# Performance work log

Measured on AMD Instinct MI355X. Metric: run time of the kernel, lower is better.

Reference implementation:

```python
import jax, jax.numpy as jnp
import numpy as np

B, H, W, C = 64, 224, 224, 32

def setup_inputs() -> dict:
    key = jax.random.key(0)
    k1, k2, k3 = jax.random.split(key, 3)
    x = jax.random.normal(k1, (B, H, W, C), dtype=jnp.float32)
    # Dense(4) params: kernel [C, 4], bias [4] (keras glorot-ish scale)
    W_cls = jax.random.normal(k2, (C, 4), dtype=jnp.float32) * (1.0 / np.sqrt(C))
    b_cls = jax.random.normal(k3, (4,), dtype=jnp.float32) * 0.01
    return {"x": x, "W_cls": W_cls, "b_cls": b_cls}

def reference(x, W_cls, b_cls):
    # mean-pool over spatial dims -> [B, C]
    mean_features = jnp.mean(x, axis=(1, 2))
    logits = mean_features @ W_cls + b_cls          # [B, 4]
    k = jnp.argmax(logits, axis=-1)                 # [B] int32
    # tf.image.rot90 rotates counter-clockwise; jnp.rot90(axes=(1,2)) matches.
    # Vectorized routing: materialize all 4 rotations, gather per-sample by k.
    rots = jnp.stack([
        x,
        jnp.rot90(x, 1, axes=(1, 2)),
        jnp.rot90(x, 2, axes=(1, 2)),
        jnp.rot90(x, 3, axes=(1, 2)),
    ], axis=0)                                      # [4, B, H, W, C]
    out = rots[k, jnp.arange(x.shape[0])]           # [B, H, W, C]
    return out
```

## Files before the change

kernel.cpp:

```cpp
#include <hip/hip_runtime.h>
#include <math.h>

#define B_  64
#define H_  224
#define W_  224
#define C_  32
#define HW_ (H_ * W_)

__global__ __launch_bounds__(256) void sum_kernel(const float* __restrict__ x,
                                                  float* __restrict__ sums) {
    const int blk   = blockIdx.x;
    const int b     = blk / 98;
    const int chunk = blk % 98;
    const int t     = threadIdx.x;
    const int c4    = t & 7;
    const int prow  = t >> 3;

    const float4* xb = (const float4*)(x + (size_t)b * HW_ * C_);
    const int pos0 = chunk * 512 + prow;

    float4 acc = make_float4(0.f, 0.f, 0.f, 0.f);
#pragma unroll
    for (int it = 0; it < 16; ++it) {
        const int pos = pos0 + it * 32;
        const float4 v = xb[(size_t)pos * 8 + c4];
        acc.x += v.x; acc.y += v.y; acc.z += v.z; acc.w += v.w;
    }

    __shared__ float4 s[256];
    s[t] = acc;
    __syncthreads();
#pragma unroll
    for (int stride = 128; stride >= 8; stride >>= 1) {
        if (t < stride) {
            const float4 o = s[t + stride];
            s[t].x += o.x; s[t].y += o.y; s[t].z += o.z; s[t].w += o.w;
        }
        __syncthreads();
    }
    if (t < 8) {
        const float4 v = s[t];
        atomicAdd(&sums[b * C_ + t * 4 + 0], v.x);
        atomicAdd(&sums[b * C_ + t * 4 + 1], v.y);
        atomicAdd(&sums[b * C_ + t * 4 + 2], v.z);
        atomicAdd(&sums[b * C_ + t * 4 + 3], v.w);
    }
}

__global__ void classify_kernel(const float* __restrict__ sums,
                                const float* __restrict__ Wc,
                                const float* __restrict__ bc,
                                int* __restrict__ kk) {
    const int b = threadIdx.x;
    if (b >= B_) return;
    float m[C_];
    const float inv = 1.0f / (float)HW_;
#pragma unroll
    for (int c = 0; c < C_; ++c) m[c] = sums[b * C_ + c] * inv;

    float best = -INFINITY;
    int bi = 0;
#pragma unroll
    for (int j = 0; j < 4; ++j) {
        float l = bc[j];
#pragma unroll
        for (int c = 0; c < C_; ++c) l += m[c] * Wc[c * 4 + j];
        if (l > best) { best = l; bi = j; }
    }
    kk[b] = bi;
}

__global__ __launch_bounds__(256) void rotate_kernel(const float* __restrict__ x,
                                                     const int* __restrict__ kk,
                                                     float* __restrict__ out) {
    const int blk = blockIdx.x;
    const int b = blk / H_;
    const int i = blk % H_;
    const int k = kk[b];

    const float4* xb = (const float4*)(x + (size_t)b * HW_ * C_);
    float4* ob = (float4*)(out + ((size_t)b * HW_ + (size_t)i * W_) * C_);

    const int t = threadIdx.x;
#pragma unroll
    for (int rep = 0; rep < 7; ++rep) {
        const int idx = rep * 256 + t;
        const int j  = idx >> 3;
        const int c4 = idx & 7;
        int si, sj;
        switch (k) {
            case 0:  si = i;          sj = j;          break;
            case 1:  si = j;          sj = W_ - 1 - i; break;
            case 2:  si = H_ - 1 - i; sj = W_ - 1 - j; break;
            default: si = H_ - 1 - j; sj = i;          break;
        }
        ob[idx] = xb[((size_t)si * W_ + sj) * 8 + c4];
    }
}

extern "C" void kernel_launch(void* const* d_in, const int* in_sizes, int n_in,
                              void* d_out, int out_size, void* d_ws, size_t ws_size,
                              hipStream_t stream) {
    const float* x   = (const float*)d_in[0];
    const float* Wc  = (const float*)d_in[1];
    const float* bc  = (const float*)d_in[2];
    float* out       = (float*)d_out;

    float* sums = (float*)d_ws;
    int*   kk   = (int*)((char*)d_ws + B_ * C_ * 4);

    hipMemsetAsync(sums, 0, B_ * C_ * sizeof(float), stream);

    sum_kernel<<<B_ * 98, 256, 0, stream>>>(x, sums);
    classify_kernel<<<1, 64, 0, stream>>>(sums, Wc, bc, kk);
    rotate_kernel<<<B_ * H_, 256, 0, stream>>>(x, kk, out);
}
```

Measured before the change: 751.1 us.

## Tile rotate kernel through shared memory and reverse batch order

Rotation now loads 16x16 pixel tiles into shared memory and writes them out rotated, so global reads and writes are both contiguous runs of pixels instead of row-strided single-pixel accesses. Batches are also processed in reverse order so the data the sum kernel touched last may still be in cache. This adds a barrier and possible LDS bank conflicts.

```diff
diff --git a/kernel.cpp b/kernel.cpp
--- a/kernel.cpp
+++ b/kernel.cpp
@@ -6,6 +6,8 @@
 #define W_  224
 #define C_  32
 #define HW_ (H_ * W_)
+#define T_  16
+#define TILES_ (W_ / T_)
 
 __global__ __launch_bounds__(256) void sum_kernel(const float* __restrict__ x,
                                                   float* __restrict__ sums) {
@@ -73,28 +75,54 @@
 __global__ __launch_bounds__(256) void rotate_kernel(const float* __restrict__ x,
                                                      const int* __restrict__ kk,
                                                      float* __restrict__ out) {
-    const int blk = blockIdx.x;
-    const int b = blk / H_;
-    const int i = blk % H_;
-    const int k = kk[b];
+    const int blk  = blockIdx.x;
+    const int b    = (B_ - 1) - blk / (TILES_ * TILES_);
+    const int trem = blk % (TILES_ * TILES_);
+    const int ti   = trem / TILES_;
+    const int tj   = trem % TILES_;
+    const int i0   = ti * T_;
+    const int j0   = tj * T_;
+    const int k    = kk[b];
+
+    int sr0, sc0;
+    switch (k) {
+        case 0:  sr0 = i0;           sc0 = j0;           break;
+        case 1:  sr0 = j0;           sc0 = W_ - T_ - i0; break;
+        case 2:  sr0 = H_ - T_ - i0; sc0 = W_ - T_ - j0; break;
+        default: sr0 = H_ - T_ - j0; sc0 = i0;           break;
+    }
+
+    __shared__ float4 tile[T_ * T_ * 8];
 
     const float4* xb = (const float4*)(x + (size_t)b * HW_ * C_);
-    float4* ob = (float4*)(out + ((size_t)b * HW_ + (size_t)i * W_) * C_);
+    float4*       ob = (float4*)(out + (size_t)b * HW_ * C_);
 
     const int t = threadIdx.x;
+
 #pragma unroll
-    for (int rep = 0; rep < 7; ++rep) {
-        const int idx = rep * 256 + t;
-        const int j  = idx >> 3;
-        const int c4 = idx & 7;
-        int si, sj;
+    for (int rep = 0; rep < 8; ++rep) {
+        const int lidx = rep * 256 + t;
+        const int r  = lidx >> 7;
+        const int c  = (lidx >> 3) & 15;
+        const int c4 = lidx & 7;
+        tile[lidx] = xb[((size_t)(sr0 + r) * W_ + (sc0 + c)) * 8 + c4];
+    }
+    __syncthreads();
+
+#pragma unroll
+    for (int rep = 0; rep < 8; ++rep) {
+        const int oidx = rep * 256 + t;
+        const int di = oidx >> 7;
+        const int dj = (oidx >> 3) & 15;
+        const int c4 = oidx & 7;
+        int r, c;
         switch (k) {
-            case 0:  si = i;          sj = j;          break;
-            case 1:  si = j;          sj = W_ - 1 - i; break;
-            case 2:  si = H_ - 1 - i; sj = W_ - 1 - j; break;
-            default: si = H_ - 1 - j; sj = i;          break;
+            case 0:  r = di;        c = dj;        break;
+            case 1:  r = dj;        c = 15 - di;   break;
+            case 2:  r = 15 - di;   c = 15 - dj;   break;
+            default: r = 15 - dj;   c = di;        break;
         }
-        ob[idx] = xb[((size_t)si * W_ + sj) * 8 + c4];
+        ob[((size_t)(i0 + di) * W_ + (j0 + dj)) * 8 + c4] = tile[(r * 16 + c) * 8 + c4];
     }
 }
 
@@ -113,5 +141,5 @@
 
     sum_kernel<<<B_ * 98, 256, 0, stream>>>(x, sums);
     classify_kernel<<<1, 64, 0, stream>>>(sums, Wc, bc, kk);
-    rotate_kernel<<<B_ * H_, 256, 0, stream>>>(x, kk, out);
+    rotate_kernel<<<B_ * TILES_ * TILES_, 256, 0, stream>>>(x, kk, out);
 }
```

Result: no change. 744.9 us (-0.8%).
